# Optimization experiments

Measured on AMD Instinct MI355X. Metric: run time of the kernel, lower is better.

## Reference

```python
import jax, jax.numpy as jnp
import numpy as np


def setup_inputs() -> dict:
    key = jax.random.key(0)
    k1, k2, k3 = jax.random.split(key, 3)
    B, N, C, R = 256, 512, 1000, 64
    x = jax.random.normal(k1, (B, N), dtype=jnp.float32)
    # kaiming_uniform_(a=0) on weight [C, R, N]: bound = sqrt(6 / fan_in), fan_in = N
    bound = float(np.sqrt(6.0 / N))
    weight = jax.random.uniform(k2, (C, R, N), dtype=jnp.float32, minval=-bound, maxval=bound)
    # original inits bias to 0, but use random to exercise the subtraction path
    bias = jax.random.normal(k3, (C, N), dtype=jnp.float32) * 0.1
    return {"x": x, "weight": weight, "bias": bias}


def reference(x, weight, bias):
    # x: [B, N]; weight: [C, R, N]; bias: [C, N]
    # Faithful math: s_r[b, c] = W_c @ (x_b - bias_c);  out[b, c] = ||s_r[b, c]||^2
    # Fused form avoiding the [B, C, N] diff blowup:
    #   W_c (x_b - b_c) = (W x)_bc - (W b)_c
    Wx = jnp.einsum("bn,crn->bcr", x, weight)      # [B, C, R]
    Wb = jnp.einsum("cn,crn->cr", bias, weight)    # [C, R]
    s_r = Wx - Wb[None, :, :]                        # [B, C, R]
    out = jnp.sum(s_r * s_r, axis=-1)                # [B, C] squared L2 norm over r
    return out
```

## Files before the change

kernel.cpp:

```cpp
#include <hip/hip_runtime.h>
#include <hip/hip_bf16.h>

#define TB 256
#define BDIM 256
#define NDIM 512
#define CDIM 1000
#define RDIM 64
#define BK 64

typedef __attribute__((ext_vector_type(4))) float f32x4;
typedef __attribute__((ext_vector_type(8))) short bf16x8;

__device__ __forceinline__ uint32_t pk2(float lo, float hi) {
    unsigned short l = __builtin_bit_cast(unsigned short, __float2bfloat16(lo));
    unsigned short h = __builtin_bit_cast(unsigned short, __float2bfloat16(hi));
    return ((uint32_t)h << 16) | (uint32_t)l;
}

__global__ __launch_bounds__(256, 2)
void Mahalanobis_72834055405642_kernel(const float* __restrict__ x,
                                       const float* __restrict__ w,
                                       const float* __restrict__ bias,
                                       float* __restrict__ out)
{
    __shared__ alignas(16) char lds_x[BDIM * BK * 2];
    __shared__ alignas(16) char lds_w[128 * BK * 2];
    __shared__ alignas(16) float bias_lds[2 * NDIM];
    __shared__ float sb_lds[128];

    const int tid  = threadIdx.x;
    const int lane = tid & 63;
    const int wv   = tid >> 6;
    const int l15  = lane & 15;
    const int lhi  = lane >> 4;
    const int c0   = blockIdx.x * 2;

    {
        const float4 bv = reinterpret_cast<const float4*>(bias + (size_t)c0 * NDIM)[tid];
        reinterpret_cast<float4*>(bias_lds)[tid] = bv;
    }

    f32x4 acc[4][8];
    #pragma unroll
    for (int m = 0; m < 4; ++m)
        #pragma unroll
        for (int n = 0; n < 8; ++n)
            acc[m][n] = (f32x4){0.f, 0.f, 0.f, 0.f};

    const int jrow = tid >> 1;
    const int jh   = tid & 1;
    const int cl   = jrow >> 6;
    const float* wbase  = w + (size_t)(c0 + cl) * (RDIM * NDIM)
                            + (size_t)(jrow & 63) * NDIM + jh * 32;
    const float* blbase = bias_lds + cl * NDIM + jh * 32;
    const int xrow = tid >> 2;
    const int xq   = tid & 3;

    float sbp = 0.f;

    __syncthreads();

    for (int kk = 0; kk < NDIM; kk += BK) {
        #pragma unroll
        for (int p = 0; p < 4; ++p) {
            const int r = p * 64 + xrow;
            const float4* src = reinterpret_cast<const float4*>(
                x + (size_t)r * NDIM + kk + xq * 16);
            float4 v0 = src[0], v1 = src[1], v2 = src[2], v3 = src[3];
            uint4 pa = {pk2(v0.x, v0.y), pk2(v0.z, v0.w), pk2(v1.x, v1.y), pk2(v1.z, v1.w)};
            uint4 pb = {pk2(v2.x, v2.y), pk2(v2.z, v2.w), pk2(v3.x, v3.y), pk2(v3.z, v3.w)};
            const int sw = (r & 7) << 4;
            char* rowp = lds_x + r * (BK * 2);
            *reinterpret_cast<uint4*>(rowp + ((xq * 32) ^ sw))      = pa;
            *reinterpret_cast<uint4*>(rowp + ((xq * 32 + 16) ^ sw)) = pb;
        }
        {
            const float4* src = reinterpret_cast<const float4*>(wbase + kk);
            const float4* bl  = reinterpret_cast<const float4*>(blbase + kk);
            char* rowp = lds_w + jrow * (BK * 2);
            const int sw = (jrow & 7) << 4;
            #pragma unroll
            for (int i2 = 0; i2 < 4; ++i2) {
                float4 va = src[i2 * 2];
                float4 vb = src[i2 * 2 + 1];
                float4 ba = bl[i2 * 2];
                float4 bb = bl[i2 * 2 + 1];
                sbp += va.x * ba.x + va.y * ba.y + va.z * ba.z + va.w * ba.w
                     + vb.x * bb.x + vb.y * bb.y + vb.z * bb.z + vb.w * bb.w;
                uint4 pkv = {pk2(va.x, va.y), pk2(va.z, va.w),
                             pk2(vb.x, vb.y), pk2(vb.z, vb.w)};
                *reinterpret_cast<uint4*>(rowp + ((jh * 64 + i2 * 16) ^ sw)) = pkv;
            }
        }
        __syncthreads();
        #pragma unroll
        for (int ks = 0; ks < 2; ++ks) {
            bf16x8 af[4];
            bf16x8 bfr[8];
            const int swr = (l15 & 7) << 4;
            #pragma unroll
            for (int m = 0; m < 4; ++m) {
                const int row = wv * 64 + m * 16 + l15;
                af[m] = *reinterpret_cast<const bf16x8*>(
                    lds_x + row * (BK * 2) + ((ks * 64 + lhi * 16) ^ swr));
            }
            #pragma unroll
            for (int n = 0; n < 8; ++n) {
                const int row = n * 16 + l15;
                bfr[n] = *reinterpret_cast<const bf16x8*>(
                    lds_w + row * (BK * 2) + ((ks * 64 + lhi * 16) ^ swr));
            }
            #pragma unroll
            for (int m = 0; m < 4; ++m)
                #pragma unroll
                for (int n = 0; n < 8; ++n)
                    acc[m][n] = __builtin_amdgcn_mfma_f32_16x16x32_bf16(
                        af[m], bfr[n], acc[m][n], 0, 0, 0);
        }
        __syncthreads();
    }

    sbp += __shfl_xor(sbp, 1);
    if (jh == 0) sb_lds[jrow] = sbp;
    __syncthreads();

    float sb[8];
    #pragma unroll
    for (int n = 0; n < 8; ++n) sb[n] = sb_lds[n * 16 + l15];

    #pragma unroll
    for (int m = 0; m < 4; ++m) {
        #pragma unroll
        for (int rg = 0; rg < 4; ++rg) {
            float p0 = 0.f, p1 = 0.f;
            #pragma unroll
            for (int n = 0; n < 4; ++n) {
                const float d0 = acc[m][n][rg]     - sb[n];
                const float d1 = acc[m][n + 4][rg] - sb[n + 4];
                p0 += d0 * d0;
                p1 += d1 * d1;
            }
            #pragma unroll
            for (int s = 1; s < 16; s <<= 1) {
                p0 += __shfl_xor(p0, s);
                p1 += __shfl_xor(p1, s);
            }
            if (l15 == 0) {
                const int b = wv * 64 + m * 16 + lhi * 4 + rg;
                float2 o2 = {p0, p1};
                *reinterpret_cast<float2*>(out + (size_t)b * CDIM + c0) = o2;
            }
        }
    }
}

extern "C" void kernel_launch(void* const* d_in, const int* in_sizes, int n_in,
                              void* d_out, int out_size, void* d_ws, size_t ws_size,
                              hipStream_t stream) {
    const float* x    = (const float*)d_in[0];
    const float* w    = (const float*)d_in[1];
    const float* bias = (const float*)d_in[2];
    float* out = (float*)d_out;
    dim3 grid(CDIM / 2);
    dim3 block(TB);
    hipLaunchKernelGGL(Mahalanobis_72834055405642_kernel, grid, block, 0, stream,
                       x, w, bias, out);
}
```

Measured before the change: 47.99 us.

## Pre-convert x to swizzled bf16 workspace and double-buffer weight tiles

A small pre-kernel converts x to bf16 once, already in the swizzled LDS layout, and writes it to the workspace. The main kernel then streams each x tile straight into LDS with global_load_lds, so the fp32 conversion is no longer repeated by all 500 blocks. Weight tiles are double-buffered in LDS and the next tile is prefetched with nontemporal loads while MFMAs run, with setprio raised around the MFMA block. The cost is an extra kernel launch and a dependence on workspace size; a fallback kernel is kept for when the workspace is too small.

Measured after the change: 83.33 us. +73.7%, slower.

```diff
diff --git a/kernel.cpp b/kernel.cpp
--- a/kernel.cpp
+++ b/kernel.cpp
@@ -1,12 +1,12 @@
 #include <hip/hip_runtime.h>
 #include <hip/hip_bf16.h>
 
-#define TB 256
 #define BDIM 256
 #define NDIM 512
 #define CDIM 1000
 #define RDIM 64
 #define BK 64
+#define NT (NDIM / BK)
 
 typedef __attribute__((ext_vector_type(4))) float f32x4;
 typedef __attribute__((ext_vector_type(8))) short bf16x8;
@@ -17,14 +17,36 @@
     return ((uint32_t)h << 16) | (uint32_t)l;
 }
 
+__device__ __forceinline__ void gload16(const void* g, void* l) {
+    __builtin_amdgcn_global_load_lds(
+        (const __attribute__((address_space(1))) void*)g,
+        (__attribute__((address_space(3))) void*)l, 16, 0, 0);
+}
+
+__global__ __launch_bounds__(256)
+void Mahalanobis_xconv_kernel(const float* __restrict__ x, uint4* __restrict__ xws)
+{
+    const int tid = blockIdx.x * 256 + threadIdx.x;
+    const int t   = tid >> 11;
+    const int rem = tid & 2047;
+    const int row = rem >> 3;
+    const int sIn = (rem & 7) << 4;
+    const int uIn = sIn ^ ((row & 7) << 4);
+    const int col0 = t * BK + (uIn >> 1);
+    const float4* src = reinterpret_cast<const float4*>(x + (size_t)row * NDIM + col0);
+    const float4 a = src[0], b = src[1];
+    uint4 pk = {pk2(a.x, a.y), pk2(a.z, a.w), pk2(b.x, b.y), pk2(b.z, b.w)};
+    xws[tid] = pk;
+}
+
 __global__ __launch_bounds__(256, 2)
-void Mahalanobis_72834055405642_kernel(const float* __restrict__ x,
+void Mahalanobis_72834055405642_kernel(const char* __restrict__ xws,
                                        const float* __restrict__ w,
                                        const float* __restrict__ bias,
                                        float* __restrict__ out)
 {
     __shared__ alignas(16) char lds_x[BDIM * BK * 2];
-    __shared__ alignas(16) char lds_w[128 * BK * 2];
+    __shared__ alignas(16) char lds_w[2][128 * BK * 2];
     __shared__ alignas(16) float bias_lds[2 * NDIM];
     __shared__ float sb_lds[128];
 
@@ -35,10 +57,177 @@
     const int lhi  = lane >> 4;
     const int c0   = blockIdx.x * 2;
 
+    reinterpret_cast<float4*>(bias_lds)[tid] =
+        reinterpret_cast<const float4*>(bias + (size_t)c0 * NDIM)[tid];
+
+    const int jrow = tid >> 1;
+    const int jh   = tid & 1;
+    const int cl   = jrow >> 6;
+    const float* wbase  = w + (size_t)(c0 + cl) * (RDIM * NDIM)
+                            + (size_t)(jrow & 63) * NDIM + jh * 32;
+    const float* blbase = bias_lds + cl * NDIM + jh * 32;
+
+    f32x4 acc[4][8];
+    #pragma unroll
+    for (int m = 0; m < 4; ++m)
+        #pragma unroll
+        for (int n = 0; n < 8; ++n)
+            acc[m][n] = (f32x4){0.f, 0.f, 0.f, 0.f};
+
+    float sbp = 0.f;
+    const int swr = (l15 & 7) << 4;
+
     {
-        const float4 bv = reinterpret_cast<const float4*>(bias + (size_t)c0 * NDIM)[tid];
-        reinterpret_cast<float4*>(bias_lds)[tid] = bv;
-    }
+        f32x4 wr[8];
+        const f32x4* src = reinterpret_cast<const f32x4*>(wbase);
+        #pragma unroll
+        for (int i = 0; i < 8; ++i) wr[i] = __builtin_nontemporal_load(src + i);
+        #pragma unroll
+        for (int q = 0; q < 8; ++q)
+            gload16(xws + wv * 8192 + q * 1024 + lane * 16,
+                    lds_x + wv * 8192 + q * 1024);
+        __syncthreads();
+        const f32x4* bl = reinterpret_cast<const f32x4*>(blbase);
+        char* rowp = lds_w[0] + jrow * 128;
+        const int sw = (jrow & 7) << 4;
+        #pragma unroll
+        for (int i2 = 0; i2 < 4; ++i2) {
+            f32x4 va = wr[i2 * 2], vb = wr[i2 * 2 + 1];
+            f32x4 ba = bl[i2 * 2], bb = bl[i2 * 2 + 1];
+            sbp += va[0]*ba[0] + va[1]*ba[1] + va[2]*ba[2] + va[3]*ba[3]
+                 + vb[0]*bb[0] + vb[1]*bb[1] + vb[2]*bb[2] + vb[3]*bb[3];
+            uint4 pkv = {pk2(va[0], va[1]), pk2(va[2], va[3]),
+                         pk2(vb[0], vb[1]), pk2(vb[2], vb[3])};
+            *reinterpret_cast<uint4*>(rowp + ((jh * 64 + i2 * 16) ^ sw)) = pkv;
+        }
+        __syncthreads();
+    }
+
+    #pragma unroll
+    for (int t = 0; t < NT; ++t) {
+        const int cur = t & 1;
+
+        f32x4 wr[8];
+        if (t < NT - 1) {
+            const f32x4* src = reinterpret_cast<const f32x4*>(wbase + (t + 1) * BK);
+            #pragma unroll
+            for (int i = 0; i < 8; ++i) wr[i] = __builtin_nontemporal_load(src + i);
+        }
+
+        bf16x8 af[4][2];
+        #pragma unroll
+        for (int m = 0; m < 4; ++m) {
+            const int row = wv * 64 + m * 16 + l15;
+            #pragma unroll
+            for (int ks = 0; ks < 2; ++ks)
+                af[m][ks] = *reinterpret_cast<const bf16x8*>(
+                    lds_x + row * 128 + ((ks * 64 + lhi * 16) ^ swr));
+        }
+
+        asm volatile("s_waitcnt lgkmcnt(0)" ::: "memory");
+        __builtin_amdgcn_sched_barrier(0);
+        __builtin_amdgcn_s_barrier();
+        __builtin_amdgcn_sched_barrier(0);
+
+        if (t < NT - 1) {
+            #pragma unroll
+            for (int q = 0; q < 8; ++q)
+                gload16(xws + (t + 1) * 32768 + wv * 8192 + q * 1024 + lane * 16,
+                        lds_x + wv * 8192 + q * 1024);
+        }
+
+        #pragma unroll
+        for (int ks = 0; ks < 2; ++ks) {
+            bf16x8 bfr[8];
+            #pragma unroll
+            for (int n = 0; n < 8; ++n) {
+                const int row = n * 16 + l15;
+                bfr[n] = *reinterpret_cast<const bf16x8*>(
+                    lds_w[cur] + row * 128 + ((ks * 64 + lhi * 16) ^ swr));
+            }
+            __builtin_amdgcn_s_setprio(1);
+            #pragma unroll
+            for (int m = 0; m < 4; ++m)
+                #pragma unroll
+                for (int n = 0; n < 8; ++n)
+                    acc[m][n] = __builtin_amdgcn_mfma_f32_16x16x32_bf16(
+                        af[m][ks], bfr[n], acc[m][n], 0, 0, 0);
+            __builtin_amdgcn_s_setprio(0);
+        }
+
+        if (t < NT - 1) {
+            const f32x4* bl = reinterpret_cast<const f32x4*>(blbase + (t + 1) * BK);
+            char* rowp = lds_w[cur ^ 1] + jrow * 128;
+            const int sw = (jrow & 7) << 4;
+            #pragma unroll
+            for (int i2 = 0; i2 < 4; ++i2) {
+                f32x4 va = wr[i2 * 2], vb = wr[i2 * 2 + 1];
+                f32x4 ba = bl[i2 * 2], bb = bl[i2 * 2 + 1];
+                sbp += va[0]*ba[0] + va[1]*ba[1] + va[2]*ba[2] + va[3]*ba[3]
+                     + vb[0]*bb[0] + vb[1]*bb[1] + vb[2]*bb[2] + vb[3]*bb[3];
+                uint4 pkv = {pk2(va[0], va[1]), pk2(va[2], va[3]),
+                             pk2(vb[0], vb[1]), pk2(vb[2], vb[3])};
+                *reinterpret_cast<uint4*>(rowp + ((jh * 64 + i2 * 16) ^ sw)) = pkv;
+            }
+        }
+
+        __syncthreads();
+    }
+
+    sbp += __shfl_xor(sbp, 1);
+    if (jh == 0) sb_lds[jrow] = sbp;
+    __syncthreads();
+
+    float sb[8];
+    #pragma unroll
+    for (int n = 0; n < 8; ++n) sb[n] = sb_lds[n * 16 + l15];
+
+    #pragma unroll
+    for (int m = 0; m < 4; ++m) {
+        #pragma unroll
+        for (int rg = 0; rg < 4; ++rg) {
+            float p0 = 0.f, p1 = 0.f;
+            #pragma unroll
+            for (int n = 0; n < 4; ++n) {
+                const float d0 = acc[m][n][rg]     - sb[n];
+                const float d1 = acc[m][n + 4][rg] - sb[n + 4];
+                p0 += d0 * d0;
+                p1 += d1 * d1;
+            }
+            #pragma unroll
+            for (int s = 1; s < 16; s <<= 1) {
+                p0 += __shfl_xor(p0, s);
+                p1 += __shfl_xor(p1, s);
+            }
+            if (l15 == 0) {
+                const int b = wv * 64 + m * 16 + lhi * 4 + rg;
+                float2 o2 = {p0, p1};
+                *reinterpret_cast<float2*>(out + (size_t)b * CDIM + c0) = o2;
+            }
+        }
+    }
+}
+
+__global__ __launch_bounds__(256, 2)
+void Mahalanobis_fallback_kernel(const float* __restrict__ x,
+                                 const float* __restrict__ w,
+                                 const float* __restrict__ bias,
+                                 float* __restrict__ out)
+{
+    __shared__ alignas(16) char lds_x[BDIM * BK * 2];
+    __shared__ alignas(16) char lds_w[128 * BK * 2];
+    __shared__ alignas(16) float bias_lds[2 * NDIM];
+    __shared__ float sb_lds[128];
+
+    const int tid  = threadIdx.x;
+    const int lane = tid & 63;
+    const int wv   = tid >> 6;
+    const int l15  = lane & 15;
+    const int lhi  = lane >> 4;
+    const int c0   = blockIdx.x * 2;
+
+    reinterpret_cast<float4*>(bias_lds)[tid] =
+        reinterpret_cast<const float4*>(bias + (size_t)c0 * NDIM)[tid];
 
     f32x4 acc[4][8];
     #pragma unroll
@@ -57,7 +246,6 @@
     const int xq   = tid & 3;
 
     float sbp = 0.f;
-
     __syncthreads();
 
     for (int kk = 0; kk < NDIM; kk += BK) {
@@ -161,8 +349,14 @@
     const float* w    = (const float*)d_in[1];
     const float* bias = (const float*)d_in[2];
     float* out = (float*)d_out;
-    dim3 grid(CDIM / 2);
-    dim3 block(TB);
-    hipLaunchKernelGGL(Mahalanobis_72834055405642_kernel, grid, block, 0, stream,
-                       x, w, bias, out);
-}
+
+    if (ws_size >= (size_t)(BDIM * NDIM * 2)) {
+        hipLaunchKernelGGL(Mahalanobis_xconv_kernel, dim3(64), dim3(256), 0, stream,
+                           x, (uint4*)d_ws);
+        hipLaunchKernelGGL(Mahalanobis_72834055405642_kernel, dim3(CDIM / 2), dim3(256),
+                           0, stream, (const char*)d_ws, w, bias, out);
+    } else {
+        hipLaunchKernelGGL(Mahalanobis_fallback_kernel, dim3(CDIM / 2), dim3(256),
+                           0, stream, x, w, bias, out);
+    }
+}
```
